# Kernel tuning notes

Hardware: AMD Instinct MI355X
Metric: run time of the kernel (lower is better)

The kernel has to match this reference:

```python
import jax, jax.numpy as jnp
import numpy as np

# ---- static config (matches init_kwargs) ----
D_MODEL = 2048
D_STATE = 64
D_CONV = 4
EXPAND = 2
HEADDIM = 64
NGROUPS = 1
CHUNK = 256
D_INNER = EXPAND * D_MODEL            # 4096
NHEADS = D_INNER // HEADDIM           # 64
CONV_DIM = D_INNER + 2 * NGROUPS * D_STATE   # 4224
D_IN_PROJ = 2 * D_INNER + 2 * NGROUPS * D_STATE + NHEADS  # 8384
EPS = 1e-5


def setup_inputs() -> dict:
    key = jax.random.key(0)
    ks = jax.random.split(key, 7)
    B, L = 2, 2048
    u = jax.random.normal(ks[0], (B, L, D_MODEL), jnp.float32)
    W_in = jax.random.normal(ks[1], (D_IN_PROJ, D_MODEL), jnp.float32) * (D_MODEL ** -0.5)
    conv_w = jax.random.normal(ks[2], (CONV_DIM, D_CONV), jnp.float32) * (D_CONV ** -0.5)
    conv_b = jnp.zeros((CONV_DIM,), jnp.float32)
    # dt_bias = softplus^{-1}(dt) with dt ~ LogUniform(1e-3, 1e-1), as in the torch init
    dt = jnp.exp(jax.random.uniform(ks[3], (NHEADS,), jnp.float32)
                 * (np.log(0.1) - np.log(0.001)) + np.log(0.001))
    dt_bias = dt + jnp.log(-jnp.expm1(-dt))
    A_log = jnp.log(jax.random.uniform(ks[4], (NHEADS,), jnp.float32, minval=1.0, maxval=16.0))
    D = jnp.ones((NHEADS,), jnp.float32)
    norm_w = jnp.ones((D_INNER,), jnp.float32)
    W_out = jax.random.normal(ks[5], (D_MODEL, D_INNER), jnp.float32) * (D_INNER ** -0.5)
    return dict(u=u, W_in=W_in, conv_w=conv_w, conv_b=conv_b, dt_bias=dt_bias,
                A_log=A_log, D=D, norm_w=norm_w, W_out=W_out)


def _chunked_ssd(x, dt, A, Bm, Cm):
    """Mamba2 chunked selective scan (ssd, discrete form).
    x:[b,l,h,p] dt:[b,l,h] A:[h] Bm,Cm:[b,l,n] (ngroups=1, broadcast over heads).
    Returns y:[b,l,h,p]."""
    b, l, h, p = x.shape
    c = l // CHUNK
    xc = x.reshape(b, c, CHUNK, h, p)
    dtc = dt.reshape(b, c, CHUNK, h)
    Bc = Bm.reshape(b, c, CHUNK, D_STATE)
    Cc = Cm.reshape(b, c, CHUNK, D_STATE)

    Abar = (dtc * A).transpose(0, 3, 1, 2)          # [b,h,c,s]
    Acum = jnp.cumsum(Abar, axis=-1)                # [b,h,c,s]

    # intra-chunk decay matrix L[i,j] = exp(sum_{k=j+1..i} Abar_k), lower-tri
    seg = Acum[..., :, None] - Acum[..., None, :]   # [b,h,c,s,s]
    tri = jnp.tril(jnp.ones((CHUNK, CHUNK), bool))
    Lmat = jnp.where(tri, jnp.exp(seg), 0.0)

    xdt = xc * dtc[..., None]                       # [b,c,s,h,p] (dt*B*x discretization)
    Y_diag = jnp.einsum('bcln,bcsn,bhcls,bcshp->bclhp', Cc, Bc, Lmat, xdt)

    # per-chunk final states
    decay_states = jnp.exp(Acum[..., -1:] - Acum)   # [b,h,c,s]
    states = jnp.einsum('bcsn,bhcs,bcshp->bchpn', Bc, decay_states, xdt)

    # inter-chunk recurrence (associative scan across chunk summaries)
    Achunk = Acum[..., -1]                          # [b,h,c]
    Acs = jnp.cumsum(jnp.pad(Achunk, ((0, 0), (0, 0), (1, 0))), axis=-1)  # [b,h,c+1]
    segc = Acs[..., :, None] - Acs[..., None, :]
    tric = jnp.tril(jnp.ones((c + 1, c + 1), bool))
    decay_chunk = jnp.where(tric, jnp.exp(segc), 0.0)          # [b,h,c+1,c+1]
    states0 = jnp.pad(states, ((0, 0), (1, 0), (0, 0), (0, 0), (0, 0)))  # zero init state
    new_states = jnp.einsum('bhzc,bchpn->bzhpn', decay_chunk, states0)
    prev_states = new_states[:, :-1]                # state entering each chunk [b,c,h,p,n]

    state_decay = jnp.exp(Acum)                     # [b,h,c,s]
    Y_off = jnp.einsum('bcln,bchpn,bhcl->bclhp', Cc, prev_states, state_decay)
    return (Y_diag + Y_off).reshape(b, l, h, p)


def reference(u, W_in, conv_w, conv_b, dt_bias, A_log, D, norm_w, W_out):
    b, l, _ = u.shape
    zxbcdt = u @ W_in.T                                        # [b,l,8384]
    z = zxbcdt[..., :D_INNER]
    xBC = zxbcdt[..., D_INNER:D_INNER + CONV_DIM]
    dt = jax.nn.softplus(zxbcdt[..., D_INNER + CONV_DIM:] + dt_bias)  # [b,l,h]

    # causal depthwise conv1d + SiLU
    xp = jnp.pad(xBC, ((0, 0), (D_CONV - 1, 0), (0, 0)))
    xBC = conv_b + sum(xp[:, w:w + l, :] * conv_w[:, w] for w in range(D_CONV))
    xBC = jax.nn.silu(xBC)

    x = xBC[..., :D_INNER].reshape(b, l, NHEADS, HEADDIM)
    Bm = xBC[..., D_INNER:D_INNER + D_STATE]
    Cm = xBC[..., D_INNER + D_STATE:]

    A = -jnp.exp(A_log)                                        # [h]
    y = _chunked_ssd(x, dt, A, Bm, Cm)                         # [b,l,h,p]
    y = y + x * D[None, None, :, None]                         # D skip on raw x
    y = y.reshape(b, l, D_INNER)

    # gated RMSNorm (norm_before_gate=False): gate first, then normalize
    y = y * jax.nn.silu(z)
    y = y * jax.lax.rsqrt(jnp.mean(y * y, axis=-1, keepdims=True) + EPS) * norm_w
    return y @ W_out.T
```

## Files before the change

### kernel.cpp

```cpp
#include <hip/hip_runtime.h>
#include <hip/hip_bf16.h>
#include <cstdint>

#define DPROJ  8384

typedef __attribute__((ext_vector_type(8))) short short8;
typedef __attribute__((ext_vector_type(4))) short sh4;
typedef __attribute__((ext_vector_type(4))) float f32x4;

#define ZX_OFF     0ul
#define DTB_OFF    34340864ul
#define ACU_OFF    34603008ul
#define CBT_OFF    34865152ul
#define ST_OFF     36175872ul
#define YB_OFF     40370176ul
#define HALO_OFF   57147392ul
#define U16_OFF    40370176ul
#define WIN16_OFF  48758784ul
#define WOUT16_OFF 34340864ul

__device__ __forceinline__ short f2bf(float x) {
  union { float f; uint32_t u; } v{x};
  uint32_t r = (v.u + 0x7fff + ((v.u >> 16) & 1)) >> 16;
  return (short)r;
}
__device__ __forceinline__ float bf2f(short s) {
  union { uint32_t u; float f; } v;
  v.u = ((uint32_t)(uint16_t)s) << 16;
  return v.f;
}

__global__ __launch_bounds__(256) void cast_bf16_kernel(
    const float* __restrict__ in, short* __restrict__ out, int n8) {
  int i = blockIdx.x * 256 + threadIdx.x;
  if (i >= n8) return;
  const float4* p = (const float4*)(in + (size_t)i * 8);
  float4 a = p[0], b = p[1];
  short8 o;
  o[0] = f2bf(a.x); o[1] = f2bf(a.y); o[2] = f2bf(a.z); o[3] = f2bf(a.w);
  o[4] = f2bf(b.x); o[5] = f2bf(b.y); o[6] = f2bf(b.z); o[7] = f2bf(b.w);
  *(short8*)(out + (size_t)i * 8) = o;
}

__device__ __forceinline__ void gload16(const void* g, const void* l) {
  __builtin_amdgcn_global_load_lds(
      (const __attribute__((address_space(1))) void*)g,
      (__attribute__((address_space(3))) void*)l, 16, 0, 0);
}

__global__ __launch_bounds__(256) void gemm_bf16(
    const short* __restrict__ A, int lda, const short* __restrict__ B, int ldb,
    float* __restrict__ C, int ldc, int K, int Nvalid) {
  const int orig = blockIdx.x + gridDim.x * blockIdx.y;
  const int xcd = orig & 7;
  const int cid = orig >> 3;
  const int rpx = gridDim.y >> 3;
  const int tn = cid / rpx;
  const int tm = xcd * rpx + (cid % rpx);
  __shared__ __align__(16) short As[128 * 32];
  __shared__ __align__(16) short Bs[128 * 32];
  const int t = threadIdx.x;
  const int w = t >> 6, lane = t & 63;
  const int m0 = tm * 128, n0 = tn * 128;
  const int wr = (w >> 1) * 64, wc = (w & 1) * 64;
  const int arow = t >> 2, kk = (t & 3) * 8;
  const int fr = lane & 15, fk = (lane >> 4) * 8;
  int br0 = n0 + arow;       if (br0 > Nvalid - 1) br0 = Nvalid - 1;
  int br1 = n0 + 64 + arow;  if (br1 > Nvalid - 1) br1 = Nvalid - 1;
  const short* pa0 = A + (size_t)(m0 + arow) * lda + kk;
  const short* pa1 = A + (size_t)(m0 + 64 + arow) * lda + kk;
  const short* pb0 = B + (size_t)br0 * ldb + kk;
  const short* pb1 = B + (size_t)br1 * ldb + kk;
  short* la = As + w * 512;
  short* lb = Bs + w * 512;
  f32x4 acc[4][4];
#pragma unroll
  for (int i = 0; i < 4; ++i)
#pragma unroll
    for (int j = 0; j < 4; ++j) acc[i][j] = (f32x4){0.f, 0.f, 0.f, 0.f};

  for (int k0 = 0; k0 < K; k0 += 32) {
    gload16(pa0 + k0, la);
    gload16(pa1 + k0, la + 2048);
    gload16(pb0 + k0, lb);
    gload16(pb1 + k0, lb + 2048);
    __syncthreads();
    short8 af[4], bg[4];
#pragma unroll
    for (int i = 0; i < 4; ++i) {
      af[i] = *(const short8*)&As[(wr + i * 16 + fr) * 32 + fk];
      bg[i] = *(const short8*)&Bs[(wc + i * 16 + fr) * 32 + fk];
    }
#pragma unroll
    for (int i = 0; i < 4; ++i)
#pragma unroll
      for (int j = 0; j < 4; ++j)
        acc[i][j] = __builtin_amdgcn_mfma_f32_16x16x32_bf16(af[i], bg[j],
                                                            acc[i][j], 0, 0, 0);
    __syncthreads();
  }
#pragma unroll
  for (int i = 0; i < 4; ++i) {
    const int row = m0 + wr + i * 16 + (lane >> 4) * 4;
#pragma unroll
    for (int j = 0; j < 4; ++j) {
      const int col = n0 + wc + j * 16 + fr;
      if (col < Nvalid) {
#pragma unroll
        for (int r = 0; r < 4; ++r)
          C[(size_t)(row + r) * ldc + col] = acc[i][j][r];
      }
    }
  }
}

__global__ __launch_bounds__(256) void halo_kernel(const float* __restrict__ zx,
                                                   float* __restrict__ halo) {
  int idx = blockIdx.x * 256 + threadIdx.x;
  int ch = idx % 4224;
  int r = idx / 4224;
  int j = r % 3;
  int r2 = r / 3;
  int lc = r2 & 15, b = r2 >> 4;
  int l = lc * 128 - 3 + j;
  halo[idx] = (l < 0) ? 0.f : zx[(size_t)(b * 2048 + l) * DPROJ + 4096 + ch];
}

__global__ __launch_bounds__(256) void conv_kernel(float* __restrict__ zx,
                                                   const float* __restrict__ halo,
                                                   const float* __restrict__ cw,
                                                   const float* __restrict__ cb) {
  int idx = blockIdx.x * 256 + threadIdx.x;
  int ch = idx % 4224;
  int r = idx / 4224;
  int lc = r & 15, b = r >> 4;
  float w0 = cw[ch * 4 + 0], w1 = cw[ch * 4 + 1], w2 = cw[ch * 4 + 2],
        w3 = cw[ch * 4 + 3];
  float bias = cb[ch];
  const float* hp = halo + (size_t)r * 3 * 4224 + ch;
  float x3 = hp[0], x2 = hp[4224], x1 = hp[2 * 4224];
  size_t base = (size_t)(b * 2048 + lc * 128) * DPROJ + 4096 + ch;
  for (int i = 0; i < 128; ++i) {
    float x0 = zx[base];
    float v = bias + w0 * x3 + w1 * x2 + w2 * x1 + w3 * x0;
    v = v / (1.f + __expf(-v));
    zx[base] = v;
    x3 = x2; x2 = x1; x1 = x0;
    base += DPROJ;
  }
}

__global__ __launch_bounds__(256) void dtacum_kernel(
    const float* __restrict__ zx, const float* __restrict__ dt_bias,
    const float* __restrict__ A_log, float* __restrict__ dtb,
    float* __restrict__ acu) {
  int bid = blockIdx.x;
  int c = bid & 7, h = (bid >> 3) & 63, b = bid >> 9;
  int s = threadIdx.x;
  int tok = b * 2048 + c * 256 + s;
  float raw = zx[(size_t)tok * DPROJ + 8320 + h] + dt_bias[h];
  float dtv = (raw > 20.f) ? raw : log1pf(expf(raw));
  float A = -expf(A_log[h]);
  __shared__ float sc[256];
  sc[s] = dtv * A;
  __syncthreads();
  for (int off = 1; off < 256; off <<= 1) {
    float v = (s >= off) ? sc[s - off] : 0.f;
    __syncthreads();
    sc[s] += v;
    __syncthreads();
  }
  int o = (b * 64 + h) * 2048 + c * 256 + s;
  dtb[o] = dtv;
  acu[o] = sc[s];
}

__global__ __launch_bounds__(256) void cbt_kernel(const float* __restrict__ zx,
                                                  short* __restrict__ cbtT) {
  __shared__ float cl[256][33];
  __shared__ float blds[16][32];
  int bid = blockIdx.x;
  int sb = bid & 15, c = (bid >> 4) & 7, b = bid >> 7;
  int t = threadIdx.x;
  int tok0 = b * 2048 + c * 256;
  float acc[16];
#pragma unroll
  for (int i = 0; i < 16; ++i) acc[i] = 0.f;
  for (int nh = 0; nh < 2; ++nh) {
    __syncthreads();
    for (int it = 0; it < 32; ++it) {
      int e = it * 256 + t;
      int row = e >> 5, n = e & 31;
      cl[row][n] = zx[(size_t)(tok0 + row) * DPROJ + 8256 + nh * 32 + n];
    }
    for (int it = 0; it < 2; ++it) {
      int e = it * 256 + t;
      int row = e >> 5, n = e & 31;
      blds[row][n] =
          zx[(size_t)(tok0 + sb * 16 + row) * DPROJ + 8192 + nh * 32 + n];
    }
    __syncthreads();
    for (int n = 0; n < 32; ++n) {
      float cv = cl[t][n];
#pragma unroll
      for (int s2 = 0; s2 < 16; ++s2) acc[s2] += cv * blds[s2][n];
    }
  }
  short* outp = cbtT + ((size_t)(b * 8 + c) * 256 + t) * 256 + sb * 16;
#pragma unroll
  for (int s2 = 0; s2 < 16; ++s2) outp[s2] = f2bf(acc[s2]);
}

__global__ __launch_bounds__(256) void states_mfma(
    const float* __restrict__ zx, const float* __restrict__ dtb,
    const float* __restrict__ acu, float* __restrict__ st) {
  __shared__ __align__(16) short As2[64][136];
  __shared__ __align__(16) short Bs2[64][136];
  __shared__ float wl[256];
  int bid = blockIdx.x;
  int h = bid & 63, c = (bid >> 6) & 7, b = bid >> 9;
  int t = threadIdx.x;
  int w = t >> 6, lane = t & 63;
  int tok0 = b * 2048 + c * 256;
  int bh = (b * 64 + h) * 2048 + c * 256;
  {
    float aend = acu[bh + 255];
    wl[t] = __expf(aend - acu[bh + t]) * dtb[bh + t];
  }
  __syncthreads();
  const float* xbase = zx + (size_t)tok0 * DPROJ + 4096 + h * 64;
  const float* bbase = zx + (size_t)tok0 * DPROJ + 8192;
  const int fr = lane & 15, fko = (lane >> 4) * 8;
  const int wi = (w >> 1) * 32, wj = (w & 1) * 32;
  f32x4 acc[2][2];
#pragma unroll
  for (int i = 0; i < 2; ++i)
#pragma unroll
    for (int j = 0; j < 2; ++j) acc[i][j] = (f32x4){0.f, 0.f, 0.f, 0.f};

  for (int ph = 0; ph < 2; ++ph) {
    const int kb = ph * 128;
    if (ph) __syncthreads();
    for (int it = 0; it < 8; ++it) {
      int idx = it * 256 + t;
      int p = idx & 63, kg = idx >> 6;
      int k = kb + kg * 4;
      const float* xp = xbase + (size_t)k * DPROJ + p;
      const float* bp = bbase + (size_t)k * DPROJ + p;
      sh4 oa, ob;
#pragma unroll
      for (int r = 0; r < 4; ++r) {
        oa[r] = f2bf(xp[(size_t)r * DPROJ]);
        ob[r] = f2bf(bp[(size_t)r * DPROJ] * wl[k + r]);
      }
      *(sh4*)&As2[p][kg * 4] = oa;
      *(sh4*)&Bs2[p][kg * 4] = ob;
    }
    __syncthreads();
#pragma unroll
    for (int kk0 = 0; kk0 < 128; kk0 += 32) {
      short8 af[2], bg[2];
#pragma unroll
      for (int i = 0; i < 2; ++i) {
        af[i] = *(const short8*)&As2[wi + i * 16 + fr][kk0 + fko];
        bg[i] = *(const short8*)&Bs2[wj + i * 16 + fr][kk0 + fko];
      }
#pragma unroll
      for (int i = 0; i < 2; ++i)
#pragma unroll
        for (int j = 0; j < 2; ++j)
          acc[i][j] = __builtin_amdgcn_mfma_f32_16x16x32_bf16(af[i], bg[j],
                                                              acc[i][j], 0, 0, 0);
    }
  }
  float* out = st + ((size_t)(b * 8 + c) * 64 + h) * 4096;
  const int rq = (lane >> 4) * 4;
#pragma unroll
  for (int i = 0; i < 2; ++i) {
    int p0 = wi + i * 16 + rq;
#pragma unroll
    for (int j = 0; j < 2; ++j) {
      int n = wj + j * 16 + fr;
#pragma unroll
      for (int r = 0; r < 4; ++r)
        out[(size_t)(p0 + r) * 64 + n] = acc[i][j][r];
    }
  }
}

__global__ __launch_bounds__(256) void chunkscan_kernel(
    const float* __restrict__ acu, float* __restrict__ st) {
  int bid = blockIdx.x;
  int pc = bid & 15, h = (bid >> 4) & 63, b = bid >> 10;
  int pn = pc * 256 + threadIdx.x;
  int abase = (b * 64 + h) * 2048;
  float run = 0.f;
  for (int c = 0; c < 8; ++c) {
    size_t idx = ((size_t)(b * 8 + c) * 64 + h) * 4096 + pn;
    float s = st[idx];
    st[idx] = run;
    float ach = acu[abase + c * 256 + 255];
    run = run * __expf(ach) + s;
  }
}

__global__ __launch_bounds__(256) void ydiag_mfma(
    const float* __restrict__ zx, const float* __restrict__ dtb,
    const float* __restrict__ acu, const short* __restrict__ cbtT,
    const float* __restrict__ st, const float* __restrict__ Dp,
    float* __restrict__ yb) {
  __shared__ __align__(16) short Xs[64][328];
  __shared__ float acs[256];
  __shared__ float dts[256];
  int bid = blockIdx.x;
  int h = bid & 63, c = (bid >> 6) & 7, b = bid >> 9;
  int t = threadIdx.x;
  int w = t >> 6, lane = t & 63;
  int tok0 = b * 2048 + c * 256;
  int bh = (b * 64 + h) * 2048 + c * 256;
  acs[t] = acu[bh + t];
  dts[t] = dtb[bh + t];
  const float* xbase = zx + (size_t)tok0 * DPROJ + 4096 + h * 64;
  const float* st_b = st + ((size_t)(b * 8 + c) * 64 + h) * 4096;
  for (int it = 0; it < 16; ++it) {
    int idx = it * 256 + t;
    int p = idx & 63, kg = idx >> 6;
    const float* xp = xbase + (size_t)(kg * 4) * DPROJ + p;
    sh4 o;
    o[0] = f2bf(xp[0]);
    o[1] = f2bf(xp[DPROJ]);
    o[2] = f2bf(xp[2 * DPROJ]);
    o[3] = f2bf(xp[3 * DPROJ]);
    *(sh4*)&Xs[p][kg * 4] = o;
  }
  for (int it = 0; it < 4; ++it) {
    int idx = it * 256 + t;
    int ng = idx & 15, p = idx >> 4;
    float4 v = *(const float4*)&st_b[p * 64 + ng * 4];
    sh4 o;
    o[0] = f2bf(v.x); o[1] = f2bf(v.y); o[2] = f2bf(v.z); o[3] = f2bf(v.w);
    *(sh4*)&Xs[p][256 + ng * 4] = o;
  }
  __syncthreads();

  const int fr = lane & 15, fko = (lane >> 4) * 8;
  const int wr = w * 64;
  float Al[4], eAl[4];
#pragma unroll
  for (int i = 0; i < 4; ++i) {
    Al[i] = acs[wr + i * 16 + fr];
    eAl[i] = __expf(Al[i]);
  }
  f32x4 acc[4][4];
#pragma unroll
  for (int i = 0; i < 4; ++i)
#pragma unroll
    for (int j = 0; j < 4; ++j) acc[i][j] = (f32x4){0.f, 0.f, 0.f, 0.f};

  const short* cbt_b = cbtT + (size_t)(b * 8 + c) * 65536;

  for (int k0 = 0; k0 < wr + 64; k0 += 32) {
    short8 bg[4];
#pragma unroll
    for (int j = 0; j < 4; ++j)
      bg[j] = *(const short8*)&Xs[j * 16 + fr][k0 + fko];
    const int bi = (k0 + 32 < 256) ? (k0 + 32) : 255;
    const float base = acs[bi];
    float vd[8];
#pragma unroll
    for (int jj = 0; jj < 8; ++jj) {
      int s = k0 + fko + jj;
      vd[jj] = __expf(base - acs[s]) * dts[s];
    }
#pragma unroll
    for (int i = 0; i < 4; ++i) {
      const int li0 = wr + i * 16;
      if (k0 > li0 + 15) continue;
      const int l = li0 + fr;
      const short8 cb = *(const short8*)&cbt_b[(size_t)l * 256 + k0 + fko];
      short8 af;
      if (k0 + 32 <= li0) {
        const float u = __expf(Al[i] - base);
#pragma unroll
        for (int jj = 0; jj < 8; ++jj)
          af[jj] = f2bf(bf2f(cb[jj]) * (vd[jj] * u));
      } else {
#pragma unroll
        for (int jj = 0; jj < 8; ++jj) {
          int s = k0 + fko + jj;
          float wv = 0.f;
          if (s <= l) wv = bf2f(cb[jj]) * __expf(Al[i] - acs[s]) * dts[s];
          af[jj] = f2bf(wv);
        }
      }
#pragma unroll
      for (int j = 0; j < 4; ++j)
        acc[i][j] = __builtin_amdgcn_mfma_f32_16x16x32_bf16(af, bg[j],
                                                            acc[i][j], 0, 0, 0);
    }
  }
#pragma unroll
  for (int k0 = 256; k0 < 320; k0 += 32) {
    short8 bg[4];
#pragma unroll
    for (int j = 0; j < 4; ++j)
      bg[j] = *(const short8*)&Xs[j * 16 + fr][k0 + fko];
#pragma unroll
    for (int i = 0; i < 4; ++i) {
      const int l = wr + i * 16 + fr;
      const float* cr =
          zx + (size_t)(tok0 + l) * DPROJ + 8256 + (k0 - 256) + fko;
      float4 c0 = *(const float4*)cr;
      float4 c1 = *(const float4*)(cr + 4);
      short8 af;
      af[0] = f2bf(c0.x * eAl[i]); af[1] = f2bf(c0.y * eAl[i]);
      af[2] = f2bf(c0.z * eAl[i]); af[3] = f2bf(c0.w * eAl[i]);
      af[4] = f2bf(c1.x * eAl[i]); af[5] = f2bf(c1.y * eAl[i]);
      af[6] = f2bf(c1.z * eAl[i]); af[7] = f2bf(c1.w * eAl[i]);
#pragma unroll
      for (int j = 0; j < 4; ++j)
        acc[i][j] = __builtin_amdgcn_mfma_f32_16x16x32_bf16(af, bg[j],
                                                            acc[i][j], 0, 0, 0);
    }
  }
  float Dh = Dp[h];
  const int rq = (lane >> 4) * 4;
#pragma unroll
  for (int i = 0; i < 4; ++i) {
    int l0 = wr + i * 16 + rq;
#pragma unroll
    for (int j = 0; j < 4; ++j) {
      int p = j * 16 + fr;
      sh4 x4 = *(const sh4*)&Xs[p][l0];
      f32x4 a = acc[i][j];
#pragma unroll
      for (int r = 0; r < 4; ++r)
        yb[(size_t)(bh + l0 + r) * 64 + p] = a[r] + Dh * bf2f(x4[r]);
    }
  }
}

__global__ __launch_bounds__(256) void gatenorm_kernel(
    const float* zx, const float* __restrict__ nw,
    const float* __restrict__ yb, short* ybh) {
  int tok = blockIdx.x;
  int b = tok >> 11, l = tok & 2047;
  int t = threadIdx.x;
  float g[16];
  float ss = 0.f;
#pragma unroll
  for (int i = 0; i < 16; ++i) {
    int d = i * 256 + t;
    int h = d >> 6, p = d & 63;
    float yv = yb[((size_t)(b * 64 + h) * 2048 + l) * 64 + p];
    float zv = zx[(size_t)tok * DPROJ + d];
    float gv = yv * (zv / (1.f + __expf(-zv)));
    g[i] = gv;
    ss += gv * gv;
  }
  for (int off = 32; off > 0; off >>= 1) ss += __shfl_down(ss, off);
  __shared__ float red[4];
  int wid = t >> 6, lane = t & 63;
  if (lane == 0) red[wid] = ss;
  __syncthreads();
  float tot = red[0] + red[1] + red[2] + red[3];
  float scale = rsqrtf(tot * (1.f / 4096.f) + 1e-5f);
#pragma unroll
  for (int i = 0; i < 16; ++i) {
    int d = i * 256 + t;
    ybh[(size_t)tok * 16768 + d] = f2bf(g[i] * scale * nw[d]);
  }
}

extern "C" void kernel_launch(void* const* d_in, const int* in_sizes, int n_in,
                              void* d_out, int out_size, void* d_ws,
                              size_t ws_size, hipStream_t stream) {
  const float* u = (const float*)d_in[0];
  const float* W_in = (const float*)d_in[1];
  const float* conv_w = (const float*)d_in[2];
  const float* conv_b = (const float*)d_in[3];
  const float* dt_bias = (const float*)d_in[4];
  const float* A_log = (const float*)d_in[5];
  const float* Dp = (const float*)d_in[6];
  const float* norm_w = (const float*)d_in[7];
  const float* W_out = (const float*)d_in[8];
  float* out = (float*)d_out;
  float* ws = (float*)d_ws;

  float* zx = ws + ZX_OFF;
  float* dtb = ws + DTB_OFF;
  float* acu = ws + ACU_OFF;
  short* cbtT = (short*)(ws + CBT_OFF);
  float* st = ws + ST_OFF;
  float* yb = ws + YB_OFF;
  float* halo = ws + HALO_OFF;
  short* u16 = (short*)(ws + U16_OFF);
  short* win16 = (short*)(ws + WIN16_OFF);
  short* wout16 = (short*)(ws + WOUT16_OFF);
  short* ybh = (short*)zx;

  cast_bf16_kernel<<<4096, 256, 0, stream>>>(u, u16, 1048576);
  cast_bf16_kernel<<<8384, 256, 0, stream>>>(W_in, win16, 2146304);
  gemm_bf16<<<dim3(66, 32), 256, 0, stream>>>(u16, 2048, win16, 2048, zx, DPROJ,
                                              2048, DPROJ);
  halo_kernel<<<1584, 256, 0, stream>>>(zx, halo);
  conv_kernel<<<528, 256, 0, stream>>>(zx, halo, conv_w, conv_b);
  dtacum_kernel<<<1024, 256, 0, stream>>>(zx, dt_bias, A_log, dtb, acu);
  cbt_kernel<<<256, 256, 0, stream>>>(zx, cbtT);
  states_mfma<<<1024, 256, 0, stream>>>(zx, dtb, acu, st);
  chunkscan_kernel<<<2048, 256, 0, stream>>>(acu, st);
  ydiag_mfma<<<1024, 256, 0, stream>>>(zx, dtb, acu, cbtT, st, Dp, yb);
  cast_bf16_kernel<<<4096, 256, 0, stream>>>(W_out, wout16, 1048576);
  gatenorm_kernel<<<4096, 256, 0, stream>>>(zx, norm_w, yb, ybh);
  gemm_bf16<<<dim3(16, 32), 256, 0, stream>>>(ybh, 16768, wout16, 4096, out,
                                              2048, 4096, 2048);
}
```

Measured before the change: 514.5 us.

## Store in-projection output as bf16 and propagate bf16 through downstream kernels

The in-projection GEMM now writes its output as bf16 instead of fp32. Halo, conv, dt, CB, states, ydiag and gatenorm kernels all read that bf16 buffer, and the gatenorm result is written in place for the output GEMM. This halves the memory traffic on the large intermediate buffer and removes several conversions. In exchange, precision drops because the pre-conv activations, z, dt, B and C values are now rounded to bf16.

```diff
diff --git a/kernel.cpp b/kernel.cpp
--- a/kernel.cpp
+++ b/kernel.cpp
@@ -8,16 +8,16 @@
 typedef __attribute__((ext_vector_type(4))) short sh4;
 typedef __attribute__((ext_vector_type(4))) float f32x4;
 
-#define ZX_OFF     0ul
-#define DTB_OFF    34340864ul
-#define ACU_OFF    34603008ul
-#define CBT_OFF    34865152ul
-#define ST_OFF     36175872ul
-#define YB_OFF     40370176ul
-#define HALO_OFF   57147392ul
-#define U16_OFF    40370176ul
-#define WIN16_OFF  48758784ul
-#define WOUT16_OFF 34340864ul
+#define ZX16_OFF   0ul
+#define DTB_OFF    17170432ul
+#define ACU_OFF    17432576ul
+#define CBT_OFF    17694720ul
+#define ST_OFF     18219008ul
+#define YB_OFF     22413312ul
+#define HALO_OFF   39190528ul
+#define U16_OFF    39393280ul
+#define WIN16_OFF  43587584ul
+#define WOUT16_OFF 39393280ul
 
 __device__ __forceinline__ short f2bf(float x) {
   union { float f; uint32_t u; } v{x};
@@ -48,9 +48,10 @@
       (__attribute__((address_space(3))) void*)l, 16, 0, 0);
 }
 
+template <int OUTBF>
 __global__ __launch_bounds__(256) void gemm_bf16(
     const short* __restrict__ A, int lda, const short* __restrict__ B, int ldb,
-    float* __restrict__ C, int ldc, int K, int Nvalid) {
+    void* __restrict__ Cv, int ldc, int K, int Nvalid) {
   const int orig = blockIdx.x + gridDim.x * blockIdx.y;
   const int xcd = orig & 7;
   const int cid = orig >> 3;
@@ -107,15 +108,19 @@
       const int col = n0 + wc + j * 16 + fr;
       if (col < Nvalid) {
 #pragma unroll
-        for (int r = 0; r < 4; ++r)
-          C[(size_t)(row + r) * ldc + col] = acc[i][j][r];
+        for (int r = 0; r < 4; ++r) {
+          if (OUTBF)
+            ((short*)Cv)[(size_t)(row + r) * ldc + col] = f2bf(acc[i][j][r]);
+          else
+            ((float*)Cv)[(size_t)(row + r) * ldc + col] = acc[i][j][r];
+        }
       }
     }
   }
 }
 
-__global__ __launch_bounds__(256) void halo_kernel(const float* __restrict__ zx,
-                                                   float* __restrict__ halo) {
+__global__ __launch_bounds__(256) void halo_kernel(const short* __restrict__ zx,
+                                                   short* __restrict__ halo) {
   int idx = blockIdx.x * 256 + threadIdx.x;
   int ch = idx % 4224;
   int r = idx / 4224;
@@ -123,11 +128,11 @@
   int r2 = r / 3;
   int lc = r2 & 15, b = r2 >> 4;
   int l = lc * 128 - 3 + j;
-  halo[idx] = (l < 0) ? 0.f : zx[(size_t)(b * 2048 + l) * DPROJ + 4096 + ch];
-}
-
-__global__ __launch_bounds__(256) void conv_kernel(float* __restrict__ zx,
-                                                   const float* __restrict__ halo,
+  halo[idx] = (l < 0) ? (short)0 : zx[(size_t)(b * 2048 + l) * DPROJ + 4096 + ch];
+}
+
+__global__ __launch_bounds__(256) void conv_kernel(short* __restrict__ zx,
+                                                   const short* __restrict__ halo,
                                                    const float* __restrict__ cw,
                                                    const float* __restrict__ cb) {
   int idx = blockIdx.x * 256 + threadIdx.x;
@@ -137,28 +142,28 @@
   float w0 = cw[ch * 4 + 0], w1 = cw[ch * 4 + 1], w2 = cw[ch * 4 + 2],
         w3 = cw[ch * 4 + 3];
   float bias = cb[ch];
-  const float* hp = halo + (size_t)r * 3 * 4224 + ch;
-  float x3 = hp[0], x2 = hp[4224], x1 = hp[2 * 4224];
+  const short* hp = halo + (size_t)r * 3 * 4224 + ch;
+  float x3 = bf2f(hp[0]), x2 = bf2f(hp[4224]), x1 = bf2f(hp[2 * 4224]);
   size_t base = (size_t)(b * 2048 + lc * 128) * DPROJ + 4096 + ch;
   for (int i = 0; i < 128; ++i) {
-    float x0 = zx[base];
+    float x0 = bf2f(zx[base]);
     float v = bias + w0 * x3 + w1 * x2 + w2 * x1 + w3 * x0;
     v = v / (1.f + __expf(-v));
-    zx[base] = v;
+    zx[base] = f2bf(v);
     x3 = x2; x2 = x1; x1 = x0;
     base += DPROJ;
   }
 }
 
 __global__ __launch_bounds__(256) void dtacum_kernel(
-    const float* __restrict__ zx, const float* __restrict__ dt_bias,
+    const short* __restrict__ zx, const float* __restrict__ dt_bias,
     const float* __restrict__ A_log, float* __restrict__ dtb,
     float* __restrict__ acu) {
   int bid = blockIdx.x;
   int c = bid & 7, h = (bid >> 3) & 63, b = bid >> 9;
   int s = threadIdx.x;
   int tok = b * 2048 + c * 256 + s;
-  float raw = zx[(size_t)tok * DPROJ + 8320 + h] + dt_bias[h];
+  float raw = bf2f(zx[(size_t)tok * DPROJ + 8320 + h]) + dt_bias[h];
   float dtv = (raw > 20.f) ? raw : log1pf(expf(raw));
   float A = -expf(A_log[h]);
   __shared__ float sc[256];
@@ -175,7 +180,7 @@
   acu[o] = sc[s];
 }
 
-__global__ __launch_bounds__(256) void cbt_kernel(const float* __restrict__ zx,
+__global__ __launch_bounds__(256) void cbt_kernel(const short* __restrict__ zx,
                                                   short* __restrict__ cbtT) {
   __shared__ float cl[256][33];
   __shared__ float blds[16][32];
@@ -191,13 +196,13 @@
     for (int it = 0; it < 32; ++it) {
       int e = it * 256 + t;
       int row = e >> 5, n = e & 31;
-      cl[row][n] = zx[(size_t)(tok0 + row) * DPROJ + 8256 + nh * 32 + n];
+      cl[row][n] = bf2f(zx[(size_t)(tok0 + row) * DPROJ + 8256 + nh * 32 + n]);
     }
     for (int it = 0; it < 2; ++it) {
       int e = it * 256 + t;
       int row = e >> 5, n = e & 31;
       blds[row][n] =
-          zx[(size_t)(tok0 + sb * 16 + row) * DPROJ + 8192 + nh * 32 + n];
+          bf2f(zx[(size_t)(tok0 + sb * 16 + row) * DPROJ + 8192 + nh * 32 + n]);
     }
     __syncthreads();
     for (int n = 0; n < 32; ++n) {
@@ -212,7 +217,7 @@
 }
 
 __global__ __launch_bounds__(256) void states_mfma(
-    const float* __restrict__ zx, const float* __restrict__ dtb,
+    const short* __restrict__ zx, const float* __restrict__ dtb,
     const float* __restrict__ acu, float* __restrict__ st) {
   __shared__ __align__(16) short As2[64][136];
   __shared__ __align__(16) short Bs2[64][136];
@@ -228,8 +233,8 @@
     wl[t] = __expf(aend - acu[bh + t]) * dtb[bh + t];
   }
   __syncthreads();
-  const float* xbase = zx + (size_t)tok0 * DPROJ + 4096 + h * 64;
-  const float* bbase = zx + (size_t)tok0 * DPROJ + 8192;
+  const short* xbase = zx + (size_t)tok0 * DPROJ + 4096 + h * 64;
+  const short* bbase = zx + (size_t)tok0 * DPROJ + 8192;
   const int fr = lane & 15, fko = (lane >> 4) * 8;
   const int wi = (w >> 1) * 32, wj = (w & 1) * 32;
   f32x4 acc[2][2];
@@ -245,13 +250,13 @@
       int idx = it * 256 + t;
       int p = idx & 63, kg = idx >> 6;
       int k = kb + kg * 4;
-      const float* xp = xbase + (size_t)k * DPROJ + p;
-      const float* bp = bbase + (size_t)k * DPROJ + p;
+      const short* xp = xbase + (size_t)k * DPROJ + p;
+      const short* bp = bbase + (size_t)k * DPROJ + p;
       sh4 oa, ob;
 #pragma unroll
       for (int r = 0; r < 4; ++r) {
-        oa[r] = f2bf(xp[(size_t)r * DPROJ]);
-        ob[r] = f2bf(bp[(size_t)r * DPROJ] * wl[k + r]);
+        oa[r] = xp[(size_t)r * DPROJ];
+        ob[r] = f2bf(bf2f(bp[(size_t)r * DPROJ]) * wl[k + r]);
       }
       *(sh4*)&As2[p][kg * 4] = oa;
       *(sh4*)&Bs2[p][kg * 4] = ob;
@@ -305,7 +310,7 @@
 }
 
 __global__ __launch_bounds__(256) void ydiag_mfma(
-    const float* __restrict__ zx, const float* __restrict__ dtb,
+    const short* __restrict__ zx, const float* __restrict__ dtb,
     const float* __restrict__ acu, const short* __restrict__ cbtT,
     const float* __restrict__ st, const float* __restrict__ Dp,
     float* __restrict__ yb) {
@@ -320,17 +325,17 @@
   int bh = (b * 64 + h) * 2048 + c * 256;
   acs[t] = acu[bh + t];
   dts[t] = dtb[bh + t];
-  const float* xbase = zx + (size_t)tok0 * DPROJ + 4096 + h * 64;
+  const short* xbase = zx + (size_t)tok0 * DPROJ + 4096 + h * 64;
   const float* st_b = st + ((size_t)(b * 8 + c) * 64 + h) * 4096;
   for (int it = 0; it < 16; ++it) {
     int idx = it * 256 + t;
     int p = idx & 63, kg = idx >> 6;
-    const float* xp = xbase + (size_t)(kg * 4) * DPROJ + p;
+    const short* xp = xbase + (size_t)(kg * 4) * DPROJ + p;
     sh4 o;
-    o[0] = f2bf(xp[0]);
-    o[1] = f2bf(xp[DPROJ]);
-    o[2] = f2bf(xp[2 * DPROJ]);
-    o[3] = f2bf(xp[3 * DPROJ]);
+    o[0] = xp[0];
+    o[1] = xp[DPROJ];
+    o[2] = xp[2 * DPROJ];
+    o[3] = xp[3 * DPROJ];
     *(sh4*)&Xs[p][kg * 4] = o;
   }
   for (int it = 0; it < 4; ++it) {
@@ -408,15 +413,11 @@
 #pragma unroll
     for (int i = 0; i < 4; ++i) {
       const int l = wr + i * 16 + fr;
-      const float* cr =
-          zx + (size_t)(tok0 + l) * DPROJ + 8256 + (k0 - 256) + fko;
-      float4 c0 = *(const float4*)cr;
-      float4 c1 = *(const float4*)(cr + 4);
+      const short8 cv = *(const short8*)(zx + (size_t)(tok0 + l) * DPROJ +
+                                         8256 + (k0 - 256) + fko);
       short8 af;
-      af[0] = f2bf(c0.x * eAl[i]); af[1] = f2bf(c0.y * eAl[i]);
-      af[2] = f2bf(c0.z * eAl[i]); af[3] = f2bf(c0.w * eAl[i]);
-      af[4] = f2bf(c1.x * eAl[i]); af[5] = f2bf(c1.y * eAl[i]);
-      af[6] = f2bf(c1.z * eAl[i]); af[7] = f2bf(c1.w * eAl[i]);
+#pragma unroll
+      for (int jj = 0; jj < 8; ++jj) af[jj] = f2bf(bf2f(cv[jj]) * eAl[i]);
 #pragma unroll
       for (int j = 0; j < 4; ++j)
         acc[i][j] = __builtin_amdgcn_mfma_f32_16x16x32_bf16(af, bg[j],
@@ -441,8 +442,7 @@
 }
 
 __global__ __launch_bounds__(256) void gatenorm_kernel(
-    const float* zx, const float* __restrict__ nw,
-    const float* __restrict__ yb, short* ybh) {
+    short* zx, const float* __restrict__ nw, const float* __restrict__ yb) {
   int tok = blockIdx.x;
   int b = tok >> 11, l = tok & 2047;
   int t = threadIdx.x;
@@ -453,7 +453,7 @@
     int d = i * 256 + t;
     int h = d >> 6, p = d & 63;
     float yv = yb[((size_t)(b * 64 + h) * 2048 + l) * 64 + p];
-    float zv = zx[(size_t)tok * DPROJ + d];
+    float zv = bf2f(zx[(size_t)tok * DPROJ + d]);
     float gv = yv * (zv / (1.f + __expf(-zv)));
     g[i] = gv;
     ss += gv * gv;
@@ -468,7 +468,7 @@
 #pragma unroll
   for (int i = 0; i < 16; ++i) {
     int d = i * 256 + t;
-    ybh[(size_t)tok * 16768 + d] = f2bf(g[i] * scale * nw[d]);
+    zx[(size_t)tok * DPROJ + d] = f2bf(g[i] * scale * nw[d]);
   }
 }
 
@@ -487,31 +487,30 @@
   float* out = (float*)d_out;
   float* ws = (float*)d_ws;
 
-  float* zx = ws + ZX_OFF;
+  short* zx16 = (short*)(ws + ZX16_OFF);
   float* dtb = ws + DTB_OFF;
   float* acu = ws + ACU_OFF;
   short* cbtT = (short*)(ws + CBT_OFF);
   float* st = ws + ST_OFF;
   float* yb = ws + YB_OFF;
-  float* halo = ws + HALO_OFF;
+  short* halo = (short*)(ws + HALO_OFF);
   short* u16 = (short*)(ws + U16_OFF);
   short* win16 = (short*)(ws + WIN16_OFF);
   short* wout16 = (short*)(ws + WOUT16_OFF);
-  short* ybh = (short*)zx;
 
   cast_bf16_kernel<<<4096, 256, 0, stream>>>(u, u16, 1048576);
   cast_bf16_kernel<<<8384, 256, 0, stream>>>(W_in, win16, 2146304);
-  gemm_bf16<<<dim3(66, 32), 256, 0, stream>>>(u16, 2048, win16, 2048, zx, DPROJ,
-                                              2048, DPROJ);
-  halo_kernel<<<1584, 256, 0, stream>>>(zx, halo);
-  conv_kernel<<<528, 256, 0, stream>>>(zx, halo, conv_w, conv_b);
-  dtacum_kernel<<<1024, 256, 0, stream>>>(zx, dt_bias, A_log, dtb, acu);
-  cbt_kernel<<<256, 256, 0, stream>>>(zx, cbtT);
-  states_mfma<<<1024, 256, 0, stream>>>(zx, dtb, acu, st);
+  gemm_bf16<1><<<dim3(66, 32), 256, 0, stream>>>(u16, 2048, win16, 2048, zx16,
+                                                 DPROJ, 2048, DPROJ);
+  halo_kernel<<<1584, 256, 0, stream>>>(zx16, halo);
+  conv_kernel<<<528, 256, 0, stream>>>(zx16, halo, conv_w, conv_b);
+  dtacum_kernel<<<1024, 256, 0, stream>>>(zx16, dt_bias, A_log, dtb, acu);
+  cbt_kernel<<<256, 256, 0, stream>>>(zx16, cbtT);
+  states_mfma<<<1024, 256, 0, stream>>>(zx16, dtb, acu, st);
   chunkscan_kernel<<<2048, 256, 0, stream>>>(acu, st);
-  ydiag_mfma<<<1024, 256, 0, stream>>>(zx, dtb, acu, cbtT, st, Dp, yb);
+  ydiag_mfma<<<1024, 256, 0, stream>>>(zx16, dtb, acu, cbtT, st, Dp, yb);
   cast_bf16_kernel<<<4096, 256, 0, stream>>>(W_out, wout16, 1048576);
-  gatenorm_kernel<<<4096, 256, 0, stream>>>(zx, norm_w, yb, ybh);
-  gemm_bf16<<<dim3(16, 32), 256, 0, stream>>>(ybh, 16768, wout16, 4096, out,
-                                              2048, 4096, 2048);
-}
+  gatenorm_kernel<<<4096, 256, 0, stream>>>(zx16, norm_w, yb);
+  gemm_bf16<0><<<dim3(16, 32), 256, 0, stream>>>(zx16, DPROJ, wout16, 4096, out,
+                                                 2048, 4096, 2048);
+}
```

Result: faster. 485.1 us (-5.7%).
